# Optimization experiments

Measured on AMD Instinct MI355X. Metric: run time of the kernel, lower is better.

Reference implementation:

```python
import jax, jax.numpy as jnp
import numpy as np
from jax import lax

B, T, I, H = 64, 512, 512, 512


def setup_inputs() -> dict:
    key = jax.random.key(0)
    ks = jax.random.split(key, 9)
    s_in = 1.0 / np.sqrt(I)
    s_h = 1.0 / np.sqrt(H)
    return {
        "x": jax.random.normal(ks[0], (B, T, I), dtype=jnp.float32),
        "h0_f": jnp.zeros((B, H), dtype=jnp.float32),
        "h0_b": jnp.zeros((B, H), dtype=jnp.float32),
        # cell_f params (torch Linear: y = x @ W.T + b)
        "Wxf_w": jax.random.uniform(ks[1], (H, I), jnp.float32, -s_in, s_in),
        "Wxf_b": jax.random.uniform(ks[2], (H,), jnp.float32, -s_in, s_in),
        "Whf_w": jax.random.uniform(ks[3], (H, H), jnp.float32, -s_h, s_h),
        # cell_b params
        "Wxb_w": jax.random.uniform(ks[4], (H, I), jnp.float32, -s_in, s_in),
        "Wxb_b": jax.random.uniform(ks[5], (H,), jnp.float32, -s_in, s_in),
        "Whb_w": jax.random.uniform(ks[6], (H, H), jnp.float32, -s_h, s_h),
    }


def _run_dir(x_tbi, h0, Wx_w, Wx_b, Wh_w, reverse):
    # Precompute input projections as one big GEMM (same math as per-step Linear)
    xproj = jnp.einsum("tbi,hi->tbh", x_tbi, Wx_w) + Wx_b  # (T,B,H)

    def step(h, xp):
        h = jnp.tanh(xp + h @ Wh_w.T)
        return h, h

    hT, hs = lax.scan(step, h0, xproj, reverse=reverse)
    return hT, hs  # hs in natural time order even when reverse=True


def reference(x, h0_f, h0_b, Wxf_w, Wxf_b, Whf_w, Wxb_w, Wxb_b, Whb_w):
    x_tbi = jnp.transpose(x, (1, 0, 2))  # (T,B,I)
    hT_f, hs_f = _run_dir(x_tbi, h0_f, Wxf_w, Wxf_b, Whf_w, reverse=False)
    hT_b, hs_b = _run_dir(x_tbi, h0_b, Wxb_w, Wxb_b, Whb_w, reverse=True)
    y = jnp.concatenate([hs_f, hs_b], axis=-1)  # (T,B,2H)
    y = jnp.transpose(y, (1, 0, 2))  # (B,T,2H)
    return y, hT_f, hT_b
```

## Files before the change

kernel.cpp:

```cpp
#include <hip/hip_runtime.h>

#define T_LEN 512
#define B_SZ  64
#define I_SZ  512
#define H_SZ  512

using half8   = __attribute__((ext_vector_type(8))) _Float16;
using half4   = __attribute__((ext_vector_type(4))) _Float16;
using float4v = __attribute__((ext_vector_type(4))) float;

__device__ __forceinline__ float fast_tanh(float x) {
    float e = __expf(2.0f * x);
    return 1.0f - 2.0f * __builtin_amdgcn_rcpf(e + 1.0f);
}

__global__ __launch_bounds__(256) void xproj_kernel(
    const float* __restrict__ x,
    const float* __restrict__ Wf, const float* __restrict__ bf,
    const float* __restrict__ Wb, const float* __restrict__ bb,
    _Float16* __restrict__ xp)
{
    __shared__ _Float16 Ash[8192];
    __shared__ _Float16 Bsh[8192];

    const int bid = blockIdx.x;
    const int swz = (bid & 7) * 256 + (bid >> 3);
    const int dir = swz & 1;
    const int nb  = (swz >> 1) & 3;
    const int mb  = swz >> 3;
    const int m0  = mb * 128;
    const int n0  = nb * 128;

    const float* __restrict__ W    = dir ? Wb : Wf;
    const float* __restrict__ bias = dir ? bb : bf;

    const int tid  = threadIdx.x;
    const int wv   = tid >> 6;
    const int lane = tid & 63;
    const int lm   = lane & 15;
    const int lq   = lane >> 4;
    const int wm   = wv >> 1;
    const int wn   = wv & 1;

    int rowA[4], ldsA[4];
    #pragma unroll
    for (int r = 0; r < 4; r++) {
        const int q   = r*256 + tid;
        const int row = q >> 3;
        const int khi = q & 7;
        rowA[r] = row;
        ldsA[r] = (row >> 4)*1024 + (khi*16 + ((row & 15) ^ khi))*8;
    }

    float4v acc[4][4];
    #pragma unroll
    for (int mt = 0; mt < 4; mt++)
        #pragma unroll
        for (int nt = 0; nt < 4; nt++)
            acc[mt][nt] = (float4v){0,0,0,0};

    for (int k0 = 0; k0 < I_SZ; k0 += 64) {
        float4v st[16];
        #pragma unroll
        for (int r = 0; r < 4; r++) {
            const int q   = r*256 + tid;
            const int khi = q & 7;
            const float* ga = x + (size_t)(m0 + rowA[r])*I_SZ + k0 + khi*8;
            const float* gb = W + (size_t)(n0 + rowA[r])*I_SZ + k0 + khi*8;
            st[r*2]     = *(const float4v*)ga;
            st[r*2 + 1] = *(const float4v*)(ga + 4);
            st[8 + r*2]     = *(const float4v*)gb;
            st[8 + r*2 + 1] = *(const float4v*)(gb + 4);
        }
        __syncthreads();
        #pragma unroll
        for (int r = 0; r < 4; r++) {
            half8 va, vb;
            #pragma unroll
            for (int e = 0; e < 4; e++) {
                va[e]   = (_Float16)st[r*2][e];
                va[e+4] = (_Float16)st[r*2+1][e];
                vb[e]   = (_Float16)st[8+r*2][e];
                vb[e+4] = (_Float16)st[8+r*2+1][e];
            }
            *(half8*)&Ash[ldsA[r]] = va;
            *(half8*)&Bsh[ldsA[r]] = vb;
        }
        __syncthreads();

        #pragma unroll
        for (int ks = 0; ks < 2; ks++) {
            const int khi = ks*4 + lq;
            const int go  = (khi*16 + (lm ^ khi))*8;
            half8 afr[4], bfr[4];
            #pragma unroll
            for (int mt = 0; mt < 4; mt++)
                afr[mt] = *(const half8*)&Ash[(wm*4 + mt)*1024 + go];
            #pragma unroll
            for (int nt = 0; nt < 4; nt++)
                bfr[nt] = *(const half8*)&Bsh[(wn*4 + nt)*1024 + go];
            #pragma unroll
            for (int mt = 0; mt < 4; mt++)
                #pragma unroll
                for (int nt = 0; nt < 4; nt++)
                    acc[mt][nt] = __builtin_amdgcn_mfma_f32_16x16x32_f16(
                        afr[mt], bfr[nt], acc[mt][nt], 0, 0, 0);
        }
    }

    #pragma unroll
    for (int nt = 0; nt < 4; nt++) {
        const int n  = n0 + wn*64 + nt*16 + lm;
        const float bv = bias[n];
        #pragma unroll
        for (int mt = 0; mt < 4; mt++) {
            #pragma unroll
            for (int j = 0; j < 4; j++) {
                const int m = m0 + wm*64 + mt*16 + lq*4 + j;
                const int b = m >> 9;
                const int t = m & 511;
                xp[(((size_t)dir*T_LEN + t)*B_SZ + b)*H_SZ + n] =
                    (_Float16)(acc[mt][nt][j] + bv);
            }
        }
    }
}

__global__ __launch_bounds__(512, 2) void rnn_kernel(
    const _Float16* __restrict__ xp,
    const float* __restrict__ Whf, const float* __restrict__ Whb,
    const float* __restrict__ h0f, const float* __restrict__ h0b,
    float* __restrict__ out)
{
    const int blk  = blockIdx.x;
    const int dir  = blk >> 2;
    const int b0   = (blk & 3) * 16;
    const int tid  = threadIdx.x;
    const int wv   = tid >> 6;
    const int lane = tid & 63;
    const int lq   = lane >> 4;
    const int lm   = lane & 15;

    const float* __restrict__ Wh = dir ? Whb : Whf;
    const float* __restrict__ h0 = dir ? h0b : h0f;

    __shared__ _Float16 hl[8192];
    __shared__ _Float16 wl[8][16][64][8];

    half8 bw[4][12];
    {
        const float* wr0 = Wh + ((size_t)(wv*64 + lm*4)) * H_SZ + lq*8;
        #pragma unroll
        for (int nt = 0; nt < 4; nt++) {
            const float* wr = wr0 + (size_t)nt * H_SZ;
            #pragma unroll
            for (int kt = 0; kt < 16; kt++) {
                float4v lo = *(const float4v*)(wr + kt*32);
                float4v hi = *(const float4v*)(wr + kt*32 + 4);
                half8 v;
                #pragma unroll
                for (int e = 0; e < 4; e++) { v[e] = (_Float16)lo[e]; v[e+4] = (_Float16)hi[e]; }
                if (kt < 12) bw[nt][kt] = v;
                else *(half8*)&wl[wv][nt*4 + (kt - 12)][lane][0] = v;
            }
        }
    }

    #pragma unroll
    for (int r = 0; r < 2; r++) {
        const int gi  = r*512 + tid;
        const int khi = gi >> 4;
        const int b   = gi & 15;
        const float* p = h0 + (size_t)(b0 + b)*H_SZ + khi*8;
        half8 v;
        #pragma unroll
        for (int e = 0; e < 8; e++) v[e] = (_Float16)p[e];
        *(half8*)&hl[(khi*16 + (b ^ (khi & 15))) * 8] = v;
    }
    __syncthreads();

    const _Float16* wlp = &wl[wv][0][lane][0];

    const int ts = dir ? -1 : 1;
    const int t0 = dir ? (T_LEN - 1) : 0;
    const _Float16* xpt = xp + (((size_t)dir*T_LEN + t0)*B_SZ + (b0 + lq*4))*H_SZ
                             + wv*64 + lm*4;
    const ptrdiff_t xstep = (ptrdiff_t)ts * (B_SZ * H_SZ);
    float* yb = out + ((size_t)(b0 + lq*4)*T_LEN + t0)*1024 + dir*512 + wv*64 + lm*4;
    const ptrdiff_t ystep = (ptrdiff_t)ts * 1024;

    const int khiw = wv*8 + (lm >> 1);
    const int gofs = (lm & 1) * 4;

    half4 xq[4];
    #pragma unroll
    for (int j = 0; j < 4; j++) xq[j] = *(const half4*)(xpt + j*H_SZ);

    #pragma unroll 1
    for (int s = 0; s < T_LEN; s++) {
        float4v acc[4];
        #pragma unroll
        for (int nt = 0; nt < 4; nt++)
            #pragma unroll
            for (int j = 0; j < 4; j++)
                acc[nt][j] = (float)xq[j][nt];

        if (s + 1 < T_LEN) {
            xpt += xstep;
            #pragma unroll
            for (int j = 0; j < 4; j++) xq[j] = *(const half4*)(xpt + j*H_SZ);
        }

        #pragma unroll
        for (int g = 0; g < 3; g++) {
            half8 af[4];
            #pragma unroll
            for (int i = 0; i < 4; i++) {
                const int c = (g*4 + i)*4 + lq;
                af[i] = *(const half8*)&hl[(c*16 + (lm ^ (c & 15))) * 8];
            }
            #pragma unroll
            for (int i = 0; i < 4; i++)
                #pragma unroll
                for (int nt = 0; nt < 4; nt++)
                    acc[nt] = __builtin_amdgcn_mfma_f32_16x16x32_f16(af[i], bw[nt][g*4 + i], acc[nt], 0, 0, 0);
        }
        {
            half8 af[4];
            #pragma unroll
            for (int i = 0; i < 4; i++) {
                const int c = (12 + i)*4 + lq;
                af[i] = *(const half8*)&hl[(c*16 + (lm ^ (c & 15))) * 8];
            }
            #pragma unroll
            for (int i = 0; i < 4; i++)
                #pragma unroll
                for (int nt = 0; nt < 4; nt++) {
                    half8 w = *(const half8*)(wlp + (nt*4 + i)*512);
                    acc[nt] = __builtin_amdgcn_mfma_f32_16x16x32_f16(af[i], w, acc[nt], 0, 0, 0);
                }
        }

        half4 pks[4];
        #pragma unroll
        for (int j = 0; j < 4; j++) {
            float4v v;
            #pragma unroll
            for (int nt = 0; nt < 4; nt++) v[nt] = fast_tanh(acc[nt][j]);
            __builtin_nontemporal_store(v, (float4v*)(yb + (size_t)j*(T_LEN*1024)));
            if (s == T_LEN - 1) {
                float* hp = out + 33554432 + (size_t)dir*32768
                          + (size_t)(b0 + lq*4 + j)*H_SZ + wv*64 + lm*4;
                __builtin_nontemporal_store(v, (float4v*)hp);
            }
            half4 pk;
            #pragma unroll
            for (int nt = 0; nt < 4; nt++) pk[nt] = (_Float16)v[nt];
            pks[j] = pk;
        }
        yb += ystep;

        asm volatile("s_waitcnt lgkmcnt(0)" ::: "memory");
        __builtin_amdgcn_s_barrier();

        #pragma unroll
        for (int j = 0; j < 4; j++)
            *(half4*)&hl[(khiw*16 + ((lq*4 + j) ^ (khiw & 15))) * 8 + gofs] = pks[j];

        asm volatile("s_waitcnt lgkmcnt(0)" ::: "memory");
        __builtin_amdgcn_s_barrier();
    }
}

extern "C" void kernel_launch(void* const* d_in, const int* in_sizes, int n_in,
                              void* d_out, int out_size, void* d_ws, size_t ws_size,
                              hipStream_t stream) {
    const float* x   = (const float*)d_in[0];
    const float* h0f = (const float*)d_in[1];
    const float* h0b = (const float*)d_in[2];
    const float* Wxf = (const float*)d_in[3];
    const float* bxf = (const float*)d_in[4];
    const float* Whf = (const float*)d_in[5];
    const float* Wxb = (const float*)d_in[6];
    const float* bxb = (const float*)d_in[7];
    const float* Whb = (const float*)d_in[8];
    float* out = (float*)d_out;

    _Float16* xpb = (_Float16*)d_ws;

    hipLaunchKernelGGL(xproj_kernel, dim3(2048), dim3(256), 0, stream,
                       x, Wxf, bxf, Wxb, bxb, xpb);
    hipLaunchKernelGGL(rnn_kernel, dim3(8), dim3(512), 0, stream,
                       xpb, Whf, Whb, h0f, h0b, out);
}
```

Measured before the change: 1.695 ms.

## Double-buffer RNN hidden state to drop a barrier; enlarge xproj GEMM tiles

The recurrent kernel now keeps two shared-memory hidden-state buffers, reading from one and writing the new state into the other. This removes one of the two block barriers per time step on the serial critical path, at the cost of doubling the LDS used for the hidden state. The input-projection GEMM also moves to 256x256 tiles with 512 threads and 8x4 MFMA tiles per wave, which raises data reuse but increases register pressure and lowers the block count.

```diff
diff --git a/kernel.cpp b/kernel.cpp
--- a/kernel.cpp
+++ b/kernel.cpp
@@ -14,22 +14,22 @@
     return 1.0f - 2.0f * __builtin_amdgcn_rcpf(e + 1.0f);
 }
 
-__global__ __launch_bounds__(256) void xproj_kernel(
+__global__ __launch_bounds__(512) void xproj_kernel(
     const float* __restrict__ x,
     const float* __restrict__ Wf, const float* __restrict__ bf,
     const float* __restrict__ Wb, const float* __restrict__ bb,
     _Float16* __restrict__ xp)
 {
-    __shared__ _Float16 Ash[8192];
-    __shared__ _Float16 Bsh[8192];
+    __shared__ _Float16 Ash[16384];
+    __shared__ _Float16 Bsh[16384];
 
     const int bid = blockIdx.x;
-    const int swz = (bid & 7) * 256 + (bid >> 3);
+    const int swz = (bid & 7) * 64 + (bid >> 3);
     const int dir = swz & 1;
-    const int nb  = (swz >> 1) & 3;
-    const int mb  = swz >> 3;
-    const int m0  = mb * 128;
-    const int n0  = nb * 128;
+    const int nb  = (swz >> 1) & 1;
+    const int mb  = swz >> 2;
+    const int m0  = mb * 256;
+    const int n0  = nb * 256;
 
     const float* __restrict__ W    = dir ? Wb : Wf;
     const float* __restrict__ bias = dir ? bb : bf;
@@ -39,22 +39,22 @@
     const int lane = tid & 63;
     const int lm   = lane & 15;
     const int lq   = lane >> 4;
-    const int wm   = wv >> 1;
-    const int wn   = wv & 1;
+    const int wm   = wv >> 2;
+    const int wn   = wv & 3;
 
     int rowA[4], ldsA[4];
     #pragma unroll
     for (int r = 0; r < 4; r++) {
-        const int q   = r*256 + tid;
+        const int q   = r*512 + tid;
         const int row = q >> 3;
         const int khi = q & 7;
         rowA[r] = row;
         ldsA[r] = (row >> 4)*1024 + (khi*16 + ((row & 15) ^ khi))*8;
     }
 
-    float4v acc[4][4];
-    #pragma unroll
-    for (int mt = 0; mt < 4; mt++)
+    float4v acc[8][4];
+    #pragma unroll
+    for (int mt = 0; mt < 8; mt++)
         #pragma unroll
         for (int nt = 0; nt < 4; nt++)
             acc[mt][nt] = (float4v){0,0,0,0};
@@ -63,7 +63,7 @@
         float4v st[16];
         #pragma unroll
         for (int r = 0; r < 4; r++) {
-            const int q   = r*256 + tid;
+            const int q   = r*512 + tid;
             const int khi = q & 7;
             const float* ga = x + (size_t)(m0 + rowA[r])*I_SZ + k0 + khi*8;
             const float* gb = W + (size_t)(n0 + rowA[r])*I_SZ + k0 + khi*8;
@@ -92,19 +92,18 @@
         for (int ks = 0; ks < 2; ks++) {
             const int khi = ks*4 + lq;
             const int go  = (khi*16 + (lm ^ khi))*8;
-            half8 afr[4], bfr[4];
-            #pragma unroll
-            for (int mt = 0; mt < 4; mt++)
-                afr[mt] = *(const half8*)&Ash[(wm*4 + mt)*1024 + go];
+            half8 bfr[4];
             #pragma unroll
             for (int nt = 0; nt < 4; nt++)
                 bfr[nt] = *(const half8*)&Bsh[(wn*4 + nt)*1024 + go];
             #pragma unroll
-            for (int mt = 0; mt < 4; mt++)
+            for (int mt = 0; mt < 8; mt++) {
+                half8 afr = *(const half8*)&Ash[(wm*8 + mt)*1024 + go];
                 #pragma unroll
                 for (int nt = 0; nt < 4; nt++)
                     acc[mt][nt] = __builtin_amdgcn_mfma_f32_16x16x32_f16(
-                        afr[mt], bfr[nt], acc[mt][nt], 0, 0, 0);
+                        afr, bfr[nt], acc[mt][nt], 0, 0, 0);
+            }
         }
     }
 
@@ -113,10 +112,10 @@
         const int n  = n0 + wn*64 + nt*16 + lm;
         const float bv = bias[n];
         #pragma unroll
-        for (int mt = 0; mt < 4; mt++) {
+        for (int mt = 0; mt < 8; mt++) {
             #pragma unroll
             for (int j = 0; j < 4; j++) {
-                const int m = m0 + wm*64 + mt*16 + lq*4 + j;
+                const int m = m0 + wm*128 + mt*16 + lq*4 + j;
                 const int b = m >> 9;
                 const int t = m & 511;
                 xp[(((size_t)dir*T_LEN + t)*B_SZ + b)*H_SZ + n] =
@@ -144,7 +143,7 @@
     const float* __restrict__ Wh = dir ? Whb : Whf;
     const float* __restrict__ h0 = dir ? h0b : h0f;
 
-    __shared__ _Float16 hl[8192];
+    __shared__ _Float16 hl[2][8192];
     __shared__ _Float16 wl[8][16][64][8];
 
     half8 bw[4][12];
@@ -175,7 +174,7 @@
         half8 v;
         #pragma unroll
         for (int e = 0; e < 8; e++) v[e] = (_Float16)p[e];
-        *(half8*)&hl[(khi*16 + (b ^ (khi & 15))) * 8] = v;
+        *(half8*)&hl[0][(khi*16 + (b ^ (khi & 15))) * 8] = v;
     }
     __syncthreads();
 
@@ -198,6 +197,9 @@
 
     #pragma unroll 1
     for (int s = 0; s < T_LEN; s++) {
+        const _Float16* hr = hl[s & 1];
+        _Float16*       hw = hl[(s & 1) ^ 1];
+
         float4v acc[4];
         #pragma unroll
         for (int nt = 0; nt < 4; nt++)
@@ -217,7 +219,7 @@
             #pragma unroll
             for (int i = 0; i < 4; i++) {
                 const int c = (g*4 + i)*4 + lq;
-                af[i] = *(const half8*)&hl[(c*16 + (lm ^ (c & 15))) * 8];
+                af[i] = *(const half8*)&hr[(c*16 + (lm ^ (c & 15))) * 8];
             }
             #pragma unroll
             for (int i = 0; i < 4; i++)
@@ -230,7 +232,7 @@
             #pragma unroll
             for (int i = 0; i < 4; i++) {
                 const int c = (12 + i)*4 + lq;
-                af[i] = *(const half8*)&hl[(c*16 + (lm ^ (c & 15))) * 8];
+                af[i] = *(const half8*)&hr[(c*16 + (lm ^ (c & 15))) * 8];
             }
             #pragma unroll
             for (int i = 0; i < 4; i++)
@@ -241,34 +243,27 @@
                 }
         }
 
-        half4 pks[4];
         #pragma unroll
         for (int j = 0; j < 4; j++) {
             float4v v;
             #pragma unroll
             for (int nt = 0; nt < 4; nt++) v[nt] = fast_tanh(acc[nt][j]);
+            half4 pk;
+            #pragma unroll
+            for (int nt = 0; nt < 4; nt++) pk[nt] = (_Float16)v[nt];
+            *(half4*)&hw[(khiw*16 + ((lq*4 + j) ^ (khiw & 15))) * 8 + gofs] = pk;
             __builtin_nontemporal_store(v, (float4v*)(yb + (size_t)j*(T_LEN*1024)));
             if (s == T_LEN - 1) {
                 float* hp = out + 33554432 + (size_t)dir*32768
                           + (size_t)(b0 + lq*4 + j)*H_SZ + wv*64 + lm*4;
                 __builtin_nontemporal_store(v, (float4v*)hp);
             }
-            half4 pk;
-            #pragma unroll
-            for (int nt = 0; nt < 4; nt++) pk[nt] = (_Float16)v[nt];
-            pks[j] = pk;
         }
         yb += ystep;
 
         asm volatile("s_waitcnt lgkmcnt(0)" ::: "memory");
         __builtin_amdgcn_s_barrier();
-
-        #pragma unroll
-        for (int j = 0; j < 4; j++)
-            *(half4*)&hl[(khiw*16 + ((lq*4 + j) ^ (khiw & 15))) * 8 + gofs] = pks[j];
-
-        asm volatile("s_waitcnt lgkmcnt(0)" ::: "memory");
-        __builtin_amdgcn_s_barrier();
+        __builtin_amdgcn_sched_barrier(0);
     }
 }
 
@@ -288,7 +283,7 @@
 
     _Float16* xpb = (_Float16*)d_ws;
 
-    hipLaunchKernelGGL(xproj_kernel, dim3(2048), dim3(256), 0, stream,
+    hipLaunchKernelGGL(xproj_kernel, dim3(512), dim3(512), 0, stream,
                        x, Wxf, bxf, Wxb, bxb, xpb);
     hipLaunchKernelGGL(rnn_kernel, dim3(8), dim3(512), 0, stream,
                        xpb, Whf, Whb, h0f, h0b, out);
```

New measurement: 1.741 ms. 2.7% more time.
